# Optimization experiments

Measured on AMD Instinct MI355X. Metric: run time of the kernel, lower is better.

## Reference

```python
import jax, jax.numpy as jnp
import numpy as np

NEG = -1e9
SLOPE = 0.2  # LeakyReLU negative slope, standard GAT


def _gat_layer(h_in, W, a_src, a_dst, mask, concat):
    # h_in: [N, Fin], W: [Fin, H*F], a_src/a_dst: [H, F], mask: [N, N] bool
    N = h_in.shape[0]
    H, F = a_src.shape
    h = (h_in @ W).reshape(N, H, F)                      # [N, H, F]
    es = jnp.einsum('nhf,hf->hn', h, a_src)              # [H, N]
    ed = jnp.einsum('nhf,hf->hn', h, a_dst)              # [H, N]
    e = jax.nn.leaky_relu(es[:, :, None] + ed[:, None, :], SLOPE)  # [H, N, N]
    e = jnp.where(mask[None, :, :], e, NEG)
    attn = jax.nn.softmax(e, axis=-1)                    # softmax over neighbors j
    out = jnp.einsum('hij,jhf->ihf', attn, h)            # [N, H, F]
    if concat:
        return out.reshape(N, H * F)
    return out.mean(axis=1)


def setup_inputs() -> dict:
    key = jax.random.key(0)
    ks = jax.random.split(key, 8)
    N, E, IN, HID, HEADS, OUT = 4096, 131072, 512, 64, 8, 16
    F1 = HID // HEADS
    return {
        'x': jax.random.normal(ks[0], (N, IN), jnp.float32),
        'edge_index': jax.random.randint(ks[1], (2, E), 0, N, jnp.int64),
        'W1': jax.random.normal(ks[2], (IN, HID), jnp.float32) * 0.05,
        'a1_src': jax.random.normal(ks[3], (HEADS, F1), jnp.float32) * 0.05,
        'a1_dst': jax.random.normal(ks[4], (HEADS, F1), jnp.float32) * 0.05,
        'W2': jax.random.normal(ks[5], (HID, OUT), jnp.float32) * 0.05,
        'a2_src': jax.random.normal(ks[6], (1, OUT), jnp.float32) * 0.05,
        'a2_dst': jax.random.normal(ks[7], (1, OUT), jnp.float32) * 0.05,
    }


def reference(x, edge_index, W1, a1_src, a1_dst, W2, a2_src, a2_dst):
    N = x.shape[0]
    # symmetric dense adjacency mask built by scatter, as in the torch code
    adj = jnp.zeros((N, N), jnp.float32)
    adj = adj.at[edge_index[0], edge_index[1]].set(1.0)
    adj = adj.at[edge_index[1], edge_index[0]].set(1.0)
    mask = adj > 0
    # eval mode: dropout(p=0.6) is identity
    h = _gat_layer(x, W1, a1_src, a1_dst, mask, concat=True)   # [N, 64]
    h = jax.nn.elu(h)
    h = _gat_layer(h, W2, a2_src, a2_dst, mask, concat=False)  # [N, out_dim]
    return jax.nn.log_softmax(h, axis=1)
```

## Files before the change

kernel.cpp:

```cpp
#include <hip/hip_runtime.h>
#include <hip/hip_bf16.h>
#include <stdint.h>

#define NNODES 4096
#define MASKW  (NNODES / 32)
#define IN_F   512
#define HID    64
#define OUTF   16
#define MAXNBR 1024

__global__ void scatter_edges(const int* __restrict__ ei, int E, uint32_t* __restrict__ mask) {
    int e = blockIdx.x * blockDim.x + threadIdx.x;
    if (e >= E) return;
    int u = ei[e], v = ei[E + e];
    if ((unsigned)u < NNODES && (unsigned)v < NNODES) {
        atomicOr(&mask[(size_t)u * MASKW + (v >> 5)], 1u << (v & 31));
        atomicOr(&mask[(size_t)v * MASKW + (u >> 5)], 1u << (u & 31));
    }
}

__global__ void __launch_bounds__(512) gemm1(const float* __restrict__ x, const float* __restrict__ W1,
                      const float* __restrict__ a_src, const float* __restrict__ a_dst,
                      float* __restrict__ h1, float* __restrict__ es, float* __restrict__ ed) {
    __shared__ float xs[8][IN_F];
    __shared__ float part[8][8][HID];
    int tid = threadIdx.x;
    int w = tid >> 6, f = tid & 63;
    int i0 = blockIdx.x * 8;

    const float4* xv = (const float4*)(x + (size_t)i0 * IN_F);
    float4* xsv = (float4*)&xs[0][0];
    xsv[tid] = xv[tid];
    xsv[tid + 512] = xv[tid + 512];
    __syncthreads();

    float acc[8];
#pragma unroll
    for (int r = 0; r < 8; ++r) acc[r] = 0.f;
    int k0 = w * 64;
    for (int k = k0; k < k0 + 64; k += 4) {
        float w0 = W1[(k + 0) * HID + f];
        float w1_ = W1[(k + 1) * HID + f];
        float w2 = W1[(k + 2) * HID + f];
        float w3 = W1[(k + 3) * HID + f];
#pragma unroll
        for (int r = 0; r < 8; ++r) {
            float4 xr = *(const float4*)&xs[r][k];
            acc[r] += xr.x * w0 + xr.y * w1_ + xr.z * w2 + xr.w * w3;
        }
    }
#pragma unroll
    for (int r = 0; r < 8; ++r) part[w][r][f] = acc[r];
    __syncthreads();

    {
        int r = tid >> 6, ff = tid & 63;
        float v = 0.f;
#pragma unroll
        for (int p = 0; p < 8; ++p) v += part[p][r][ff];
        h1[(size_t)(i0 + r) * HID + ff] = v;
        xs[r][ff] = v;
    }
    __syncthreads();

    if (tid < 64) {
        int r = tid >> 3, h = tid & 7;
        float s1 = 0.f, s2 = 0.f;
#pragma unroll
        for (int ff = 0; ff < 8; ++ff) {
            float hv = xs[r][h * 8 + ff];
            s1 += hv * a_src[h * 8 + ff];
            s2 += hv * a_dst[h * 8 + ff];
        }
        es[h * NNODES + (i0 + r)] = s1;
        ed[h * NNODES + (i0 + r)] = s2;
    }
}

__global__ void __launch_bounds__(512) attn1(const uint32_t* __restrict__ mask,
    const float* __restrict__ h1, const float* __restrict__ es, const float* __restrict__ ed,
    float* __restrict__ hout) {
    __shared__ int nbr[MAXNBR];
    __shared__ int cnt;
    int i = blockIdx.x;
    int tid = threadIdx.x;
    if (tid == 0) cnt = 0;
    __syncthreads();
    for (int w = tid; w < MASKW; w += 512) {
        uint32_t bits = mask[(size_t)i * MASKW + w];
        while (bits) {
            int b = __ffs(bits) - 1;
            bits &= bits - 1;
            int pos = atomicAdd(&cnt, 1);
            if (pos < MAXNBR) nbr[pos] = w * 32 + b;
        }
    }
    __syncthreads();
    int n = cnt < MAXNBR ? cnt : MAXNBR;
    int h = tid >> 6, lane = tid & 63;
    float es_i = es[h * NNODES + i];
    const float* edh = ed + h * NNODES;
    float m = -1e30f, s = 0.f;
    float acc[8];
#pragma unroll
    for (int f = 0; f < 8; ++f) acc[f] = 0.f;
    for (int t = lane; t < n; t += 64) {
        int j = nbr[t];
        float v = es_i + edh[j];
        v = v > 0.f ? v : 0.2f * v;
        float nm = fmaxf(m, v);
        float sc = __expf(m - nm);
        float p  = __expf(v - nm);
        s = s * sc + p;
        const float* hj = h1 + (size_t)j * HID + h * 8;
#pragma unroll
        for (int f = 0; f < 8; ++f) acc[f] = acc[f] * sc + p * hj[f];
        m = nm;
    }
#pragma unroll
    for (int off = 32; off >= 1; off >>= 1) {
        float mo = __shfl_xor(m, off, 64);
        float so = __shfl_xor(s, off, 64);
        float ao[8];
#pragma unroll
        for (int f = 0; f < 8; ++f) ao[f] = __shfl_xor(acc[f], off, 64);
        float nm = fmaxf(m, mo);
        float c1 = __expf(m - nm), c2 = __expf(mo - nm);
        s = s * c1 + so * c2;
#pragma unroll
        for (int f = 0; f < 8; ++f) acc[f] = acc[f] * c1 + ao[f] * c2;
        m = nm;
    }
    if (lane == 0) {
        float inv = (s > 0.f) ? 1.f / s : 0.f;
#pragma unroll
        for (int f = 0; f < 8; ++f) {
            float o = acc[f] * inv;
            o = o > 0.f ? o : (__expf(o) - 1.f);
            hout[(size_t)i * HID + h * 8 + f] = o;
        }
    }
}

__global__ void __launch_bounds__(64) gemm2(const float* __restrict__ hin, const float* __restrict__ W2,
                      const float* __restrict__ a_src, const float* __restrict__ a_dst,
                      float* __restrict__ h2, float* __restrict__ es, float* __restrict__ ed) {
    __shared__ float hs[4][HID];
    __shared__ float os[4][OUTF];
    int tid = threadIdx.x;
    int i0 = blockIdx.x * 4;
    for (int t = tid; t < 4 * HID; t += 64)
        hs[t >> 6][t & 63] = hin[(size_t)i0 * HID + t];
    __syncthreads();
    int r = tid >> 4, f = tid & 15;
    float acc = 0.f;
#pragma unroll
    for (int k = 0; k < HID; ++k) acc += hs[r][k] * W2[k * OUTF + f];
    os[r][f] = acc;
    h2[(size_t)(i0 + r) * OUTF + f] = acc;
    __syncthreads();
    if (tid < 4) {
        float s1 = 0.f, s2 = 0.f;
#pragma unroll
        for (int ff = 0; ff < OUTF; ++ff) {
            s1 += os[tid][ff] * a_src[ff];
            s2 += os[tid][ff] * a_dst[ff];
        }
        es[i0 + tid] = s1;
        ed[i0 + tid] = s2;
    }
}

__global__ void __launch_bounds__(64) attn2(const uint32_t* __restrict__ mask,
    const float* __restrict__ h2, const float* __restrict__ es, const float* __restrict__ ed,
    float* __restrict__ out) {
    __shared__ int nbr[MAXNBR];
    __shared__ int cnt;
    int i = blockIdx.x;
    int lane = threadIdx.x;
    if (lane == 0) cnt = 0;
    __syncthreads();
    for (int w = lane; w < MASKW; w += 64) {
        uint32_t bits = mask[(size_t)i * MASKW + w];
        while (bits) {
            int b = __ffs(bits) - 1;
            bits &= bits - 1;
            int pos = atomicAdd(&cnt, 1);
            if (pos < MAXNBR) nbr[pos] = w * 32 + b;
        }
    }
    __syncthreads();
    int n = cnt < MAXNBR ? cnt : MAXNBR;
    float es_i = es[i];
    float m = -1e30f, s = 0.f;
    float acc[OUTF];
#pragma unroll
    for (int f = 0; f < OUTF; ++f) acc[f] = 0.f;
    for (int t = lane; t < n; t += 64) {
        int j = nbr[t];
        float v = es_i + ed[j];
        v = v > 0.f ? v : 0.2f * v;
        float nm = fmaxf(m, v);
        float sc = __expf(m - nm);
        float p  = __expf(v - nm);
        s = s * sc + p;
        const float* hj = h2 + (size_t)j * OUTF;
#pragma unroll
        for (int f = 0; f < OUTF; ++f) acc[f] = acc[f] * sc + p * hj[f];
        m = nm;
    }
#pragma unroll
    for (int off = 32; off >= 1; off >>= 1) {
        float mo = __shfl_xor(m, off, 64);
        float so = __shfl_xor(s, off, 64);
        float ao[OUTF];
#pragma unroll
        for (int f = 0; f < OUTF; ++f) ao[f] = __shfl_xor(acc[f], off, 64);
        float nm = fmaxf(m, mo);
        float c1 = __expf(m - nm), c2 = __expf(mo - nm);
        s = s * c1 + so * c2;
#pragma unroll
        for (int f = 0; f < OUTF; ++f) acc[f] = acc[f] * c1 + ao[f] * c2;
        m = nm;
    }
    if (lane == 0) {
        float inv = (s > 0.f) ? 1.f / s : 0.f;
        float v[OUTF];
        float mx = -1e30f;
#pragma unroll
        for (int f = 0; f < OUTF; ++f) {
            v[f] = acc[f] * inv;
            mx = fmaxf(mx, v[f]);
        }
        float se = 0.f;
#pragma unroll
        for (int f = 0; f < OUTF; ++f) se += __expf(v[f] - mx);
        float lse = mx + __logf(se);
#pragma unroll
        for (int f = 0; f < OUTF; ++f)
            out[(size_t)i * OUTF + f] = v[f] - lse;
    }
}

extern "C" void kernel_launch(void* const* d_in, const int* in_sizes, int n_in,
                              void* d_out, int out_size, void* d_ws, size_t ws_size,
                              hipStream_t stream) {
    const float* x   = (const float*)d_in[0];
    const int*   ei  = (const int*)d_in[1];
    const float* W1  = (const float*)d_in[2];
    const float* a1s = (const float*)d_in[3];
    const float* a1d = (const float*)d_in[4];
    const float* W2  = (const float*)d_in[5];
    const float* a2s = (const float*)d_in[6];
    const float* a2d = (const float*)d_in[7];
    float* out = (float*)d_out;
    int E = in_sizes[1] / 2;

    char* ws = (char*)d_ws;
    uint32_t* mask = (uint32_t*)ws;
    float* h1   = (float*)(ws + 2097152);
    float* es1  = (float*)(ws + 3145728);
    float* ed1  = (float*)(ws + 3276800);
    float* hout = (float*)(ws + 3407872);
    float* h2   = (float*)(ws + 4456448);
    float* es2  = (float*)(ws + 4718592);
    float* ed2  = (float*)(ws + 4734976);

    hipMemsetAsync(mask, 0, NNODES * MASKW * sizeof(uint32_t), stream);
    scatter_edges<<<(E + 255) / 256, 256, 0, stream>>>(ei, E, mask);
    gemm1<<<NNODES / 8, 512, 0, stream>>>(x, W1, a1s, a1d, h1, es1, ed1);
    attn1<<<NNODES, 512, 0, stream>>>(mask, h1, es1, ed1, hout);
    gemm2<<<NNODES / 4, 64, 0, stream>>>(hout, W2, a2s, a2d, h2, es2, ed2);
    attn2<<<NNODES, 64, 0, stream>>>(mask, h2, es2, ed2, out);
}
```

Baseline: 134.1 us.

## Fuse layer-2 projection into attention-1 and compact neighbor lists with warp scans

Folds the second layer's linear projection and attention-score computation into the tail of the first attention kernel, which removes the gemm2 launch and the hout round-trip through global memory. Neighbor-list compaction now uses popcount plus a wavefront prefix scan instead of shared-memory atomics. Attention-2 processes four nodes per block, one wavefront each, and feature gathers use float4 loads. The neighbor cap drops from 1024 to 512. That is safe for an average degree of about 64, but any node with more than 512 neighbors would have its list truncated.

After: 133.0 us. Within noise of the previous version (-0.8%).

```diff
diff --git a/kernel.cpp b/kernel.cpp
--- a/kernel.cpp
+++ b/kernel.cpp
@@ -7,7 +7,7 @@
 #define IN_F   512
 #define HID    64
 #define OUTF   16
-#define MAXNBR 1024
+#define CAP    512
 
 __global__ void scatter_edges(const int* __restrict__ ei, int E, uint32_t* __restrict__ mask) {
     int e = blockIdx.x * blockDim.x + threadIdx.x;
@@ -77,27 +77,38 @@
     }
 }
 
-__global__ void __launch_bounds__(512) attn1(const uint32_t* __restrict__ mask,
+__global__ void __launch_bounds__(512) attn1_fused(const uint32_t* __restrict__ mask,
     const float* __restrict__ h1, const float* __restrict__ es, const float* __restrict__ ed,
-    float* __restrict__ hout) {
-    __shared__ int nbr[MAXNBR];
-    __shared__ int cnt;
+    const float* __restrict__ W2, const float* __restrict__ a2s, const float* __restrict__ a2d,
+    float* __restrict__ h2, float* __restrict__ es2, float* __restrict__ ed2) {
+    __shared__ int nbr[CAP];
+    __shared__ float hs[HID];
+    __shared__ float part[4][OUTF];
+    __shared__ int degs;
     int i = blockIdx.x;
     int tid = threadIdx.x;
-    if (tid == 0) cnt = 0;
-    __syncthreads();
-    for (int w = tid; w < MASKW; w += 512) {
-        uint32_t bits = mask[(size_t)i * MASKW + w];
-        while (bits) {
-            int b = __ffs(bits) - 1;
-            bits &= bits - 1;
-            int pos = atomicAdd(&cnt, 1);
-            if (pos < MAXNBR) nbr[pos] = w * 32 + b;
-        }
-    }
-    __syncthreads();
-    int n = cnt < MAXNBR ? cnt : MAXNBR;
     int h = tid >> 6, lane = tid & 63;
+
+    if (tid < 64) {
+        uint32_t b0 = mask[(size_t)i * MASKW + 2 * tid];
+        uint32_t b1 = mask[(size_t)i * MASKW + 2 * tid + 1];
+        int cnt = __popc(b0) + __popc(b1);
+        int incl = cnt;
+#pragma unroll
+        for (int d = 1; d < 64; d <<= 1) {
+            int t = __shfl_up(incl, d, 64);
+            if (tid >= d) incl += t;
+        }
+        int pos = incl - cnt;
+        int base = tid * 64;
+        while (b0) { int b = __ffs(b0) - 1; b0 &= b0 - 1; if (pos < CAP) nbr[pos] = base + b; ++pos; }
+        base += 32;
+        while (b1) { int b = __ffs(b1) - 1; b1 &= b1 - 1; if (pos < CAP) nbr[pos] = base + b; ++pos; }
+        if (tid == 63) degs = (incl < CAP) ? incl : CAP;
+    }
+    __syncthreads();
+    int n = degs;
+
     float es_i = es[h * NNODES + i];
     const float* edh = ed + h * NNODES;
     float m = -1e30f, s = 0.f;
@@ -112,9 +123,12 @@
         float sc = __expf(m - nm);
         float p  = __expf(v - nm);
         s = s * sc + p;
-        const float* hj = h1 + (size_t)j * HID + h * 8;
-#pragma unroll
-        for (int f = 0; f < 8; ++f) acc[f] = acc[f] * sc + p * hj[f];
+        const float4* hj = (const float4*)(h1 + (size_t)j * HID + h * 8);
+        float4 h0 = hj[0], h1v = hj[1];
+        acc[0] = acc[0] * sc + p * h0.x; acc[1] = acc[1] * sc + p * h0.y;
+        acc[2] = acc[2] * sc + p * h0.z; acc[3] = acc[3] * sc + p * h0.w;
+        acc[4] = acc[4] * sc + p * h1v.x; acc[5] = acc[5] * sc + p * h1v.y;
+        acc[6] = acc[6] * sc + p * h1v.z; acc[7] = acc[7] * sc + p * h1v.w;
         m = nm;
     }
 #pragma unroll
@@ -137,76 +151,84 @@
         for (int f = 0; f < 8; ++f) {
             float o = acc[f] * inv;
             o = o > 0.f ? o : (__expf(o) - 1.f);
-            hout[(size_t)i * HID + h * 8 + f] = o;
-        }
-    }
-}
-
-__global__ void __launch_bounds__(64) gemm2(const float* __restrict__ hin, const float* __restrict__ W2,
-                      const float* __restrict__ a_src, const float* __restrict__ a_dst,
-                      float* __restrict__ h2, float* __restrict__ es, float* __restrict__ ed) {
-    __shared__ float hs[4][HID];
-    __shared__ float os[4][OUTF];
-    int tid = threadIdx.x;
-    int i0 = blockIdx.x * 4;
-    for (int t = tid; t < 4 * HID; t += 64)
-        hs[t >> 6][t & 63] = hin[(size_t)i0 * HID + t];
-    __syncthreads();
-    int r = tid >> 4, f = tid & 15;
-    float acc = 0.f;
-#pragma unroll
-    for (int k = 0; k < HID; ++k) acc += hs[r][k] * W2[k * OUTF + f];
-    os[r][f] = acc;
-    h2[(size_t)(i0 + r) * OUTF + f] = acc;
-    __syncthreads();
-    if (tid < 4) {
+            hs[h * 8 + f] = o;
+        }
+    }
+    __syncthreads();
+
+    if (tid < 64) {
+        int q = tid >> 4, f = tid & 15;
+        float p = 0.f;
+#pragma unroll
+        for (int k = 16 * q; k < 16 * q + 16; ++k) p += hs[k] * W2[k * OUTF + f];
+        part[q][f] = p;
+    }
+    __syncthreads();
+    if (tid < OUTF) {
+        float v = part[0][tid] + part[1][tid] + part[2][tid] + part[3][tid];
+        h2[(size_t)i * OUTF + tid] = v;
+        hs[tid] = v;
+    }
+    __syncthreads();
+    if (tid == 0) {
         float s1 = 0.f, s2 = 0.f;
 #pragma unroll
-        for (int ff = 0; ff < OUTF; ++ff) {
-            s1 += os[tid][ff] * a_src[ff];
-            s2 += os[tid][ff] * a_dst[ff];
-        }
-        es[i0 + tid] = s1;
-        ed[i0 + tid] = s2;
-    }
-}
-
-__global__ void __launch_bounds__(64) attn2(const uint32_t* __restrict__ mask,
+        for (int f = 0; f < OUTF; ++f) { s1 += hs[f] * a2s[f]; s2 += hs[f] * a2d[f]; }
+        es2[i] = s1;
+        ed2[i] = s2;
+    }
+}
+
+__global__ void __launch_bounds__(256) attn2(const uint32_t* __restrict__ mask,
     const float* __restrict__ h2, const float* __restrict__ es, const float* __restrict__ ed,
     float* __restrict__ out) {
-    __shared__ int nbr[MAXNBR];
-    __shared__ int cnt;
-    int i = blockIdx.x;
-    int lane = threadIdx.x;
-    if (lane == 0) cnt = 0;
-    __syncthreads();
-    for (int w = lane; w < MASKW; w += 64) {
-        uint32_t bits = mask[(size_t)i * MASKW + w];
-        while (bits) {
-            int b = __ffs(bits) - 1;
-            bits &= bits - 1;
-            int pos = atomicAdd(&cnt, 1);
-            if (pos < MAXNBR) nbr[pos] = w * 32 + b;
-        }
-    }
-    __syncthreads();
-    int n = cnt < MAXNBR ? cnt : MAXNBR;
+    __shared__ int nbr[4][CAP];
+    int tid = threadIdx.x;
+    int wid = tid >> 6, lane = tid & 63;
+    int i = blockIdx.x * 4 + wid;
+
+    uint32_t b0 = mask[(size_t)i * MASKW + 2 * lane];
+    uint32_t b1 = mask[(size_t)i * MASKW + 2 * lane + 1];
+    int cnt = __popc(b0) + __popc(b1);
+    int incl = cnt;
+#pragma unroll
+    for (int d = 1; d < 64; d <<= 1) {
+        int t = __shfl_up(incl, d, 64);
+        if (lane >= d) incl += t;
+    }
+    int pos = incl - cnt;
+    int base = lane * 64;
+    int* myn = &nbr[wid][0];
+    while (b0) { int b = __ffs(b0) - 1; b0 &= b0 - 1; if (pos < CAP) myn[pos] = base + b; ++pos; }
+    base += 32;
+    while (b1) { int b = __ffs(b1) - 1; b1 &= b1 - 1; if (pos < CAP) myn[pos] = base + b; ++pos; }
+    int n = __shfl(incl, 63, 64);
+    n = n < CAP ? n : CAP;
+    __syncthreads();
+
     float es_i = es[i];
     float m = -1e30f, s = 0.f;
     float acc[OUTF];
 #pragma unroll
     for (int f = 0; f < OUTF; ++f) acc[f] = 0.f;
     for (int t = lane; t < n; t += 64) {
-        int j = nbr[t];
+        int j = myn[t];
         float v = es_i + ed[j];
         v = v > 0.f ? v : 0.2f * v;
         float nm = fmaxf(m, v);
         float sc = __expf(m - nm);
         float p  = __expf(v - nm);
         s = s * sc + p;
-        const float* hj = h2 + (size_t)j * OUTF;
-#pragma unroll
-        for (int f = 0; f < OUTF; ++f) acc[f] = acc[f] * sc + p * hj[f];
+        const float4* hj = (const float4*)(h2 + (size_t)j * OUTF);
+        float4 q0 = hj[0], q1 = hj[1], q2 = hj[2], q3 = hj[3];
+        acc[0]  = acc[0]  * sc + p * q0.x; acc[1]  = acc[1]  * sc + p * q0.y;
+        acc[2]  = acc[2]  * sc + p * q0.z; acc[3]  = acc[3]  * sc + p * q0.w;
+        acc[4]  = acc[4]  * sc + p * q1.x; acc[5]  = acc[5]  * sc + p * q1.y;
+        acc[6]  = acc[6]  * sc + p * q1.z; acc[7]  = acc[7]  * sc + p * q1.w;
+        acc[8]  = acc[8]  * sc + p * q2.x; acc[9]  = acc[9]  * sc + p * q2.y;
+        acc[10] = acc[10] * sc + p * q2.z; acc[11] = acc[11] * sc + p * q2.w;
+        acc[12] = acc[12] * sc + p * q3.x; acc[13] = acc[13] * sc + p * q3.y;
+        acc[14] = acc[14] * sc + p * q3.z; acc[15] = acc[15] * sc + p * q3.w;
         m = nm;
     }
 #pragma unroll
@@ -261,15 +283,13 @@
     float* h1   = (float*)(ws + 2097152);
     float* es1  = (float*)(ws + 3145728);
     float* ed1  = (float*)(ws + 3276800);
-    float* hout = (float*)(ws + 3407872);
-    float* h2   = (float*)(ws + 4456448);
-    float* es2  = (float*)(ws + 4718592);
-    float* ed2  = (float*)(ws + 4734976);
+    float* h2   = (float*)(ws + 3407872);
+    float* es2  = (float*)(ws + 3670016);
+    float* ed2  = (float*)(ws + 3686400);
 
     hipMemsetAsync(mask, 0, NNODES * MASKW * sizeof(uint32_t), stream);
     scatter_edges<<<(E + 255) / 256, 256, 0, stream>>>(ei, E, mask);
     gemm1<<<NNODES / 8, 512, 0, stream>>>(x, W1, a1s, a1d, h1, es1, ed1);
-    attn1<<<NNODES, 512, 0, stream>>>(mask, h1, es1, ed1, hout);
-    gemm2<<<NNODES / 4, 64, 0, stream>>>(hout, W2, a2s, a2d, h2, es2, ed2);
-    attn2<<<NNODES, 64, 0, stream>>>(mask, h2, es2, ed2, out);
-}
+    attn1_fused<<<NNODES, 512, 0, stream>>>(mask, h1, es1, ed1, W2, a2s, a2d, h2, es2, ed2);
+    attn2<<<NNODES / 4, 256, 0, stream>>>(mask, h2, es2, ed2, out);
+}
```
